# Kernel optimization log

Measured on AMD Instinct MI355X. Metric: run time of the kernel, lower is better.

The kernel has to match this reference:

```python
import jax, jax.numpy as jnp
import numpy as np

B, L, D = 2, 2048, 1024
H, E = 16, 64  # n_heads, per-head dim (E_q=E_k=E_v)
EPS = 1e-5


def _layernorm(x):
    # fresh nn.LayerNorm each forward: gamma=1, beta=0, eps=1e-5 (biased var)
    mu = jnp.mean(x, axis=-1, keepdims=True)
    var = jnp.mean(jnp.square(x - mu), axis=-1, keepdims=True)
    return (x - mu) * jax.lax.rsqrt(var + EPS)


def setup_inputs() -> dict:
    key = jax.random.key(0)
    ks = jax.random.split(key, 9)
    s_in = 1.0 / np.sqrt(D)
    s_ctx = 1.0 / np.sqrt(H * E)
    return {
        "query": jax.random.normal(ks[0], (B, L, D), jnp.float32),
        "key": jax.random.normal(ks[1], (B, L, D), jnp.float32),
        "value": jax.random.normal(ks[2], (B, L, D), jnp.float32),
        # torch nn.Linear weights are [out_features, in_features]
        "W_Q": jax.random.uniform(ks[3], (H * E, D), jnp.float32, -s_in, s_in),
        "W_K": jax.random.uniform(ks[4], (H * E, D), jnp.float32, -s_in, s_in),
        "W_V": jax.random.uniform(ks[5], (H * E, D), jnp.float32, -s_in, s_in),
        "W_O": jax.random.uniform(ks[6], (D, H * E), jnp.float32, -s_ctx, s_ctx),
        "fc_w": jax.random.uniform(ks[7], (D, D), jnp.float32, -s_in, s_in),
        "fc_b": jax.random.uniform(ks[8], (D,), jnp.float32, -s_in, s_in),
    }


def reference(query, key, value, W_Q, W_K, W_V, W_O, fc_w, fc_b):
    b = query.shape[0]
    # projections -> [B, H, L, E]
    q = (query @ W_Q.T).reshape(b, -1, H, E).transpose(0, 2, 1, 3)
    k = (key @ W_K.T).reshape(b, -1, H, E).transpose(0, 2, 1, 3)
    v = (value @ W_V.T).reshape(b, -1, H, E).transpose(0, 2, 1, 3)
    scores = jnp.einsum('bhqe,bhke->bhqk', q, k) / np.sqrt(E).astype(np.float32)
    A = jax.nn.softmax(scores, axis=-1)                 # [B,H,Lq,Lk]
    ctx = jnp.einsum('bhqk,bhke->bhqe', A, v)           # [B,H,L,E]
    ctx = ctx.transpose(0, 2, 1, 3).reshape(b, -1, H * E)
    attn_out = ctx @ W_O.T                               # dropout = identity (eval)
    x = _layernorm(attn_out + query)
    out = x @ fc_w.T + fc_b                              # dropout = identity (eval)
    out = _layernorm(x + out)
    return out
```

## Files before the change

kernel.cpp:

```cpp
#include <hip/hip_runtime.h>
#include <stdint.h>

typedef unsigned short u16;
typedef __bf16 bf16x8 __attribute__((ext_vector_type(8)));
typedef __bf16 bf16x4 __attribute__((ext_vector_type(4)));
typedef float f32x4 __attribute__((ext_vector_type(4)));

#define MFMA16(a,b,c) __builtin_amdgcn_mfma_f32_16x16x32_bf16((a),(b),(c),0,0,0)

__device__ __forceinline__ bf16x4 pack4(float a, float b, float c, float d){
  bf16x4 r; r[0]=(__bf16)a; r[1]=(__bf16)b; r[2]=(__bf16)c; r[3]=(__bf16)d; return r;
}

__device__ __forceinline__ void gl2lds16(const void* g, void* l){
  __builtin_amdgcn_global_load_lds(
      (const __attribute__((address_space(1))) unsigned int*)g,
      (__attribute__((address_space(3))) unsigned int*)l, 16, 0, 0);
}

__device__ __forceinline__ bf16x8 ldsfrag(const u16* base, int row, int gr){
  return *(const bf16x8*)(base + row * 64 + ((gr ^ (row & 7)) << 3));
}

template<int NB, int BN>
__device__ __forceinline__ void gemm_core(const u16* __restrict__ A,
                                          const u16* __restrict__ Bt,
                                          int N, int K, int mode,
                                          void* __restrict__ Cout,
                                          const float* __restrict__ bias,
                                          float oscale)
{
  constexpr int NF = BN / 32;
  __shared__ u16 Al[NB][128 * 64];
  __shared__ u16 Bl[NB][BN * 64];
  const int tid  = threadIdx.x;
  const int lane = tid & 63;
  const int w    = tid >> 6;
  const int wr   = w >> 1, wc = w & 1;
  const int l15  = lane & 15, g = lane >> 4;
  const int rowBase = blockIdx.y << 7;
  const int colBase = blockIdx.x * BN;

  const int srow = tid >> 3;
  const int swz  = ((tid & 7) ^ (srow & 7)) << 3;
  const u16* Ag = A  + (size_t)(rowBase + srow) * K + swz;
  const u16* Bg = Bt + (size_t)(colBase + srow) * K + swz;

  f32x4 acc[4][NF];
#pragma unroll
  for (int m = 0; m < 4; ++m)
#pragma unroll
    for (int n = 0; n < NF; ++n) acc[m][n] = f32x4{0.f, 0.f, 0.f, 0.f};

  auto stage = [&](int buf, int k0) {
#pragma unroll
    for (int i = 0; i < 4; ++i)
      gl2lds16(Ag + (size_t)(i * 32) * K + k0, Al[buf] + i * 2048 + w * 512);
#pragma unroll
    for (int i = 0; i < BN / 32; ++i)
      gl2lds16(Bg + (size_t)(i * 32) * K + k0, Bl[buf] + i * 2048 + w * 512);
  };
  auto compute = [&](int buf) {
    __builtin_amdgcn_s_setprio(1);
#pragma unroll
    for (int kk = 0; kk < 2; ++kk) {
      bf16x8 af[4], bfr[NF];
#pragma unroll
      for (int m = 0; m < 4; ++m) af[m]  = ldsfrag(Al[buf], wr * 64 + m * 16 + l15, kk * 4 + g);
#pragma unroll
      for (int n = 0; n < NF; ++n) bfr[n] = ldsfrag(Bl[buf], wc * (BN/2) + n * 16 + l15, kk * 4 + g);
#pragma unroll
      for (int m = 0; m < 4; ++m)
#pragma unroll
        for (int n = 0; n < NF; ++n)
          acc[m][n] = MFMA16(af[m], bfr[n], acc[m][n]);
    }
    __builtin_amdgcn_s_setprio(0);
  };

  if (NB == 2) {
    stage(0, 0);
    __syncthreads();
    int cur = 0;
    for (int k0 = 0; k0 < K; k0 += 64) {
      if (k0 + 64 < K) stage(cur ^ 1, k0 + 64);
      compute(cur);
      __syncthreads();
      cur ^= 1;
    }
  } else {
    for (int k0 = 0; k0 < K; k0 += 64) {
      stage(0, k0);
      __syncthreads();
      compute(0);
      __syncthreads();
    }
  }

#pragma unroll
  for (int m = 0; m < 4; ++m) {
#pragma unroll
    for (int n = 0; n < NF; ++n) {
      const int row0 = rowBase + wr * 64 + m * 16 + g * 4;
      const int col  = colBase + wc * (BN/2) + n * 16 + l15;
      if (mode == 1) {
        const int b = row0 >> 11, l = row0 & 2047;
        const int h = col >> 6,  e = col & 63;
        *(bf16x4*)((u16*)Cout + ((size_t)((((b << 4) + h) << 6) | e) << 11) + l) =
            pack4(acc[m][n][0], acc[m][n][1], acc[m][n][2], acc[m][n][3]);
      } else {
        const float bb = (mode == 4) ? bias[col] : 0.f;
#pragma unroll
        for (int r = 0; r < 4; ++r) {
          const int row = row0 + r;
          const float v = acc[m][n][r];
          if (mode == 0) {
            *(__bf16*)((u16*)Cout + (size_t)row * N + col) = (__bf16)(v * oscale);
          } else {
            *(__bf16*)((u16*)Cout + (size_t)row * N + col) = (__bf16)(v + bb);
          }
        }
      }
    }
  }
}

#define QSCALE 0.18033688011112042f

__global__ __launch_bounds__(256) void k_proj(
    const u16* __restrict__ qb, const u16* __restrict__ kb, const u16* __restrict__ vb,
    const u16* __restrict__ wq, const u16* __restrict__ wk, const u16* __restrict__ wv,
    u16* __restrict__ Qp, u16* __restrict__ Kp, u16* __restrict__ Vt)
{
  const int z = blockIdx.z;
  const u16* A = (z == 0) ? qb : (z == 1) ? kb : vb;
  const u16* B = (z == 0) ? wq : (z == 1) ? wk : wv;
  void* C = (z == 0) ? (void*)Qp : (z == 1) ? (void*)Kp : (void*)Vt;
  gemm_core<2, 64>(A, B, 1024, 1024, (z == 2) ? 1 : 0, C, nullptr, (z == 0) ? QSCALE : 1.0f);
}

__global__ __launch_bounds__(256) void k_gemm_o(const u16* __restrict__ A,
                                                const u16* __restrict__ B,
                                                u16* __restrict__ C)
{ gemm_core<2, 64>(A, B, 1024, 1024, 0, (void*)C, nullptr, 1.0f); }

__global__ __launch_bounds__(256) void k_gemm_fc(const u16* __restrict__ A,
                                                 const u16* __restrict__ B,
                                                 u16* __restrict__ C,
                                                 const float* __restrict__ bias)
{ gemm_core<2, 64>(A, B, 1024, 1024, 4, (void*)C, bias, 1.0f); }

__global__ __launch_bounds__(256, 2) void k_attn(const u16* __restrict__ Qp,
                                                 const u16* __restrict__ Kp,
                                                 const u16* __restrict__ Vt,
                                                 u16* __restrict__ ctx)
{
  __shared__ u16 Klds[3][64 * 64];
  __shared__ u16 Vlds[3][64 * 64];
  __shared__ u16 Plds[4][32 * 64];

  const int tid = threadIdx.x, lane = tid & 63, w = tid >> 6;
  const int l15 = lane & 15, g = lane >> 4, l7 = l15 & 7;
  const int bh = blockIdx.y, b = bh >> 4, h = bh & 15;
  const int q0 = blockIdx.x << 7;

  bf16x8 bq[2][2];
#pragma unroll
  for (int u = 0; u < 2; ++u) {
    const u16* Qr = Qp + (((size_t)((b << 11) + q0 + (w << 5) + (u << 4) + l15)) << 10)
                  + (h << 6) + (g << 3);
    bq[u][0] = *(const bf16x8*)(Qr);
    bq[u][1] = *(const bf16x8*)(Qr + 32);
  }

  const f32x4 zero4 = {0.f, 0.f, 0.f, 0.f};
  f32x4 o0[4], o1[4];
#pragma unroll
  for (int f = 0; f < 4; ++f) { o0[f] = zero4; o1[f] = zero4; }
  float ds0 = 0.f, ds1 = 0.f;

  const int srow = tid >> 3;
  const int swz  = ((tid & 7) ^ (srow & 7)) << 3;
  const u16* Kg = Kp + (((size_t)((b << 11) + srow)) << 10) + (h << 6) + swz;
  const u16* Vg = Vt + (((size_t)((bh << 6) + srow)) << 11) + swz;
  u16* Pw = Plds[w];

  auto stage = [&](int buf, int j0) {
#pragma unroll
    for (int i = 0; i < 2; ++i) {
      gl2lds16(Kg + ((size_t)(j0 + i * 32) << 10), Klds[buf] + i * 2048 + w * 512);
      gl2lds16(Vg + ((size_t)(i * 32) << 11) + j0, Vlds[buf] + i * 2048 + w * 512);
    }
  };

  stage(0, 0);
  stage(1, 64);
  asm volatile("s_waitcnt vmcnt(4)" ::: "memory");
  __builtin_amdgcn_s_barrier();

  int cur = 0;
  for (int t = 0; t < 32; ++t) {
    if (t + 2 < 32) {
      int nb = cur + 2; if (nb >= 3) nb -= 3;
      stage(nb, (t + 2) << 6);
    }

    bf16x8 kf[4][2];
#pragma unroll
    for (int f = 0; f < 4; ++f) {
      kf[f][0] = ldsfrag(Klds[cur], f * 16 + l15, g);
      kf[f][1] = ldsfrag(Klds[cur], f * 16 + l15, 4 + g);
    }
    f32x4 s0[4], s1[4];
    __builtin_amdgcn_s_setprio(1);
#pragma unroll
    for (int f = 0; f < 4; ++f) {
      s0[f] = MFMA16(kf[f][0], bq[0][0], zero4);
      s0[f] = MFMA16(kf[f][1], bq[0][1], s0[f]);
      s1[f] = MFMA16(kf[f][0], bq[1][0], zero4);
      s1[f] = MFMA16(kf[f][1], bq[1][1], s1[f]);
    }
    __builtin_amdgcn_s_setprio(0);

#pragma unroll
    for (int f = 0; f < 4; ++f) {
      const float a0 = __builtin_amdgcn_exp2f(s0[f][0]);
      const float a1 = __builtin_amdgcn_exp2f(s0[f][1]);
      const float a2 = __builtin_amdgcn_exp2f(s0[f][2]);
      const float a3 = __builtin_amdgcn_exp2f(s0[f][3]);
      ds0 += (a0 + a1) + (a2 + a3);
      *(bf16x4*)(Pw + l15 * 64 + ((((2 * f) + (g >> 1)) ^ l7) << 3) + ((g & 1) << 2)) =
          pack4(a0, a1, a2, a3);
      const float c0 = __builtin_amdgcn_exp2f(s1[f][0]);
      const float c1 = __builtin_amdgcn_exp2f(s1[f][1]);
      const float c2 = __builtin_amdgcn_exp2f(s1[f][2]);
      const float c3 = __builtin_amdgcn_exp2f(s1[f][3]);
      ds1 += (c0 + c1) + (c2 + c3);
      *(bf16x4*)(Pw + (16 + l15) * 64 + ((((2 * f) + (g >> 1)) ^ l7) << 3) + ((g & 1) << 2)) =
          pack4(c0, c1, c2, c3);
    }
    asm volatile("s_waitcnt lgkmcnt(0)" ::: "memory");
    __builtin_amdgcn_sched_barrier(0);

    bf16x8 vf[4][2];
#pragma unroll
    for (int f = 0; f < 4; ++f) {
      vf[f][0] = ldsfrag(Vlds[cur], f * 16 + l15, g);
      vf[f][1] = ldsfrag(Vlds[cur], f * 16 + l15, 4 + g);
    }
    __builtin_amdgcn_s_setprio(1);
#pragma unroll
    for (int kk = 0; kk < 2; ++kk) {
      const bf16x8 pb0 = *(const bf16x8*)(Pw + l15 * 64 + (((kk * 4 + g) ^ l7) << 3));
      const bf16x8 pb1 = *(const bf16x8*)(Pw + (16 + l15) * 64 + (((kk * 4 + g) ^ l7) << 3));
#pragma unroll
      for (int f = 0; f < 4; ++f) {
        o0[f] = MFMA16(vf[f][kk], pb0, o0[f]);
        o1[f] = MFMA16(vf[f][kk], pb1, o1[f]);
      }
    }
    __builtin_amdgcn_s_setprio(0);

    if (t + 2 < 32) {
      asm volatile("s_waitcnt vmcnt(4)" ::: "memory");
      __builtin_amdgcn_s_barrier();
    } else if (t + 1 < 32) {
      asm volatile("s_waitcnt vmcnt(0)" ::: "memory");
      __builtin_amdgcn_s_barrier();
    }
    ++cur; if (cur >= 3) cur -= 3;
  }

  ds0 += __shfl_xor(ds0, 16, 64);
  ds0 += __shfl_xor(ds0, 32, 64);
  ds1 += __shfl_xor(ds1, 16, 64);
  ds1 += __shfl_xor(ds1, 32, 64);
  const float i0 = 1.0f / ds0, i1 = 1.0f / ds1;
  const size_t r0 = (((size_t)((b << 11) + q0 + (w << 5) + l15)) << 10) + (h << 6);
  const size_t r1 = r0 + (16 << 10);
#pragma unroll
  for (int f = 0; f < 4; ++f) {
    *(bf16x4*)(ctx + r0 + f * 16 + (g << 2)) =
        pack4(o0[f][0] * i0, o0[f][1] * i0, o0[f][2] * i0, o0[f][3] * i0);
    *(bf16x4*)(ctx + r1 + f * 16 + (g << 2)) =
        pack4(o1[f][0] * i1, o1[f][1] * i1, o1[f][2] * i1, o1[f][3] * i1);
  }
}

__device__ __forceinline__ void ln_stats(float4 t, int tid, float& mean, float& inv){
  float s = t.x + t.y + t.z + t.w;
  float q = t.x * t.x + t.y * t.y + t.z * t.z + t.w * t.w;
#pragma unroll
  for (int d = 1; d < 64; d <<= 1) {
    s += __shfl_xor(s, d, 64);
    q += __shfl_xor(q, d, 64);
  }
  __shared__ float ps[4], pq[4];
  const int w = tid >> 6;
  if ((tid & 63) == 0) { ps[w] = s; pq[w] = q; }
  __syncthreads();
  s = ps[0] + ps[1] + ps[2] + ps[3];
  q = pq[0] + pq[1] + pq[2] + pq[3];
  mean = s * (1.0f / 1024.0f);
  const float var = q * (1.0f / 1024.0f) - mean * mean;
  inv = rsqrtf(var + 1e-5f);
}

__global__ __launch_bounds__(256) void k_ln1(const u16* __restrict__ a,
                                             const float* __restrict__ res,
                                             u16* __restrict__ xb)
{
  const int row = blockIdx.x, tid = threadIdx.x;
  const size_t base = (size_t)row << 10;
  const bf16x4 av = ((const bf16x4*)(a + base))[tid];
  const float4 rr = ((const float4*)(res + base))[tid];
  float4 t;
  t.x = (float)av[0] + rr.x; t.y = (float)av[1] + rr.y;
  t.z = (float)av[2] + rr.z; t.w = (float)av[3] + rr.w;
  float mean, inv;
  ln_stats(t, tid, mean, inv);
  ((bf16x4*)(xb + base))[tid] = pack4((t.x - mean) * inv, (t.y - mean) * inv,
                                      (t.z - mean) * inv, (t.w - mean) * inv);
}

__global__ __launch_bounds__(256) void k_ln2(const u16* __restrict__ a,
                                             const u16* __restrict__ res,
                                             float* __restrict__ out)
{
  const int row = blockIdx.x, tid = threadIdx.x;
  const size_t base = (size_t)row << 10;
  const bf16x4 av = ((const bf16x4*)(a + base))[tid];
  const bf16x4 rv = ((const bf16x4*)(res + base))[tid];
  float4 t;
  t.x = (float)av[0] + (float)rv[0]; t.y = (float)av[1] + (float)rv[1];
  t.z = (float)av[2] + (float)rv[2]; t.w = (float)av[3] + (float)rv[3];
  float mean, inv;
  ln_stats(t, tid, mean, inv);
  float4 o;
  o.x = (t.x - mean) * inv; o.y = (t.y - mean) * inv;
  o.z = (t.z - mean) * inv; o.w = (t.w - mean) * inv;
  ((float4*)(out + base))[tid] = o;
}

__global__ __launch_bounds__(256) void k_cvt3(const float* __restrict__ q,
                                              const float* __restrict__ k,
                                              const float* __restrict__ v,
                                              u16* __restrict__ qo,
                                              u16* __restrict__ ko,
                                              u16* __restrict__ vo)
{
  const int z = blockIdx.y;
  const float* src = (z == 0) ? q : (z == 1) ? k : v;
  u16* dst = (z == 0) ? qo : (z == 1) ? ko : vo;
  const int i = blockIdx.x * 256 + threadIdx.x;
  const float4 t = ((const float4*)src)[i];
  ((bf16x4*)dst)[i] = pack4(t.x, t.y, t.z, t.w);
}

__global__ __launch_bounds__(256) void k_cvt5(const float* __restrict__ a0,
                                              const float* __restrict__ a1,
                                              const float* __restrict__ a2,
                                              const float* __restrict__ a3,
                                              const float* __restrict__ a4,
                                              u16* __restrict__ o0, u16* __restrict__ o1,
                                              u16* __restrict__ o2, u16* __restrict__ o3,
                                              u16* __restrict__ o4)
{
  const int z = blockIdx.y;
  const float* src = (z == 0) ? a0 : (z == 1) ? a1 : (z == 2) ? a2 : (z == 3) ? a3 : a4;
  u16* dst = (z == 0) ? o0 : (z == 1) ? o1 : (z == 2) ? o2 : (z == 3) ? o3 : o4;
  const int i = blockIdx.x * 256 + threadIdx.x;
  const float4 t = ((const float4*)src)[i];
  ((bf16x4*)dst)[i] = pack4(t.x, t.y, t.z, t.w);
}

extern "C" void kernel_launch(void* const* d_in, const int* in_sizes, int n_in,
                              void* d_out, int out_size, void* d_ws, size_t ws_size,
                              hipStream_t stream)
{
  (void)in_sizes; (void)n_in; (void)out_size; (void)ws_size;
  const float* query = (const float*)d_in[0];
  const float* key   = (const float*)d_in[1];
  const float* value = (const float*)d_in[2];
  const float* W_Q   = (const float*)d_in[3];
  const float* W_K   = (const float*)d_in[4];
  const float* W_V   = (const float*)d_in[5];
  const float* W_O   = (const float*)d_in[6];
  const float* fc_w  = (const float*)d_in[7];
  const float* fc_b  = (const float*)d_in[8];
  float* out = (float*)d_out;
  char* ws = (char*)d_ws;

  u16*   qb    = (u16*)(ws + 0);
  u16*   kb    = (u16*)(ws + 8388608);
  u16*   vb    = (u16*)(ws + 16777216);
  u16*   wq    = (u16*)(ws + 25165824);
  u16*   wk    = (u16*)(ws + 27262976);
  u16*   wv    = (u16*)(ws + 29360128);
  u16*   wo    = (u16*)(ws + 31457280);
  u16*   fw    = (u16*)(ws + 33554432);
  u16*   Qp    = (u16*)(ws + 35651584);
  u16*   Kp    = (u16*)(ws + 44040192);
  u16*   Vt    = (u16*)(ws + 52428800);
  u16*   ctx   = (u16*)(ws + 60817408);
  u16*   attnb = (u16*)(ws + 69206016);
  u16*   xb    = vb;
  u16*   yb    = qb;

  k_cvt3<<<dim3(4096, 3), 256, 0, stream>>>(query, key, value, qb, kb, vb);
  k_cvt5<<<dim3(1024, 5), 256, 0, stream>>>(W_Q, W_K, W_V, W_O, fc_w, wq, wk, wv, wo, fw);
  k_proj<<<dim3(16, 32, 3), 256, 0, stream>>>(qb, kb, vb, wq, wk, wv, Qp, Kp, Vt);
  k_attn<<<dim3(16, 32), 256, 0, stream>>>(Qp, Kp, Vt, ctx);
  k_gemm_o<<<dim3(16, 32), 256, 0, stream>>>(ctx, wo, attnb);
  k_ln1<<<dim3(4096), 256, 0, stream>>>(attnb, query, xb);
  k_gemm_fc<<<dim3(16, 32), 256, 0, stream>>>(xb, fw, yb, fc_b);
  k_ln2<<<dim3(4096), 256, 0, stream>>>(yb, xb, out);
}
```

Before: 156.3 us.

## Split attention over two KV halves with a separate combine kernel

The attention kernel now runs a third grid dimension that splits the 2048 keys into two halves. Each half writes unnormalized fp32 partial outputs and per-row softmax denominators to a workspace buffer. A new combine kernel then sums the halves, normalizes, and writes the bf16 context. K/V staging also drops from triple to double buffering with full __syncthreads, which reduces LDS use. The aim is more blocks in flight and better CU occupancy, at the cost of an extra launch, roughly 32 MB of fp32 partial traffic, and less prefetch depth.

```diff
diff --git a/kernel.cpp b/kernel.cpp
--- a/kernel.cpp
+++ b/kernel.cpp
@@ -153,16 +153,19 @@
 __global__ __launch_bounds__(256, 2) void k_attn(const u16* __restrict__ Qp,
                                                  const u16* __restrict__ Kp,
                                                  const u16* __restrict__ Vt,
-                                                 u16* __restrict__ ctx)
-{
-  __shared__ u16 Klds[3][64 * 64];
-  __shared__ u16 Vlds[3][64 * 64];
+                                                 float* __restrict__ Opart,
+                                                 float* __restrict__ dpart)
+{
+  __shared__ u16 Klds[2][64 * 64];
+  __shared__ u16 Vlds[2][64 * 64];
   __shared__ u16 Plds[4][32 * 64];
 
   const int tid = threadIdx.x, lane = tid & 63, w = tid >> 6;
   const int l15 = lane & 15, g = lane >> 4, l7 = l15 & 7;
   const int bh = blockIdx.y, b = bh >> 4, h = bh & 15;
   const int q0 = blockIdx.x << 7;
+  const int half = blockIdx.z;
+  const int kvbase = half << 10;
 
   bf16x8 bq[2][2];
 #pragma unroll
@@ -181,8 +184,8 @@
 
   const int srow = tid >> 3;
   const int swz  = ((tid & 7) ^ (srow & 7)) << 3;
-  const u16* Kg = Kp + (((size_t)((b << 11) + srow)) << 10) + (h << 6) + swz;
-  const u16* Vg = Vt + (((size_t)((bh << 6) + srow)) << 11) + swz;
+  const u16* Kg = Kp + (((size_t)((b << 11) + kvbase + srow)) << 10) + (h << 6) + swz;
+  const u16* Vg = Vt + (((size_t)((bh << 6) + srow)) << 11) + kvbase + swz;
   u16* Pw = Plds[w];
 
   auto stage = [&](int buf, int j0) {
@@ -194,16 +197,11 @@
   };
 
   stage(0, 0);
-  stage(1, 64);
-  asm volatile("s_waitcnt vmcnt(4)" ::: "memory");
-  __builtin_amdgcn_s_barrier();
-
+  __syncthreads();
   int cur = 0;
-  for (int t = 0; t < 32; ++t) {
-    if (t + 2 < 32) {
-      int nb = cur + 2; if (nb >= 3) nb -= 3;
-      stage(nb, (t + 2) << 6);
-    }
+
+  for (int j0 = 0; j0 < 1024; j0 += 64) {
+    if (j0 + 64 < 1024) stage(cur ^ 1, j0 + 64);
 
     bf16x8 kf[4][2];
 #pragma unroll
@@ -260,31 +258,42 @@
       }
     }
     __builtin_amdgcn_s_setprio(0);
-
-    if (t + 2 < 32) {
-      asm volatile("s_waitcnt vmcnt(4)" ::: "memory");
-      __builtin_amdgcn_s_barrier();
-    } else if (t + 1 < 32) {
-      asm volatile("s_waitcnt vmcnt(0)" ::: "memory");
-      __builtin_amdgcn_s_barrier();
-    }
-    ++cur; if (cur >= 3) cur -= 3;
+    __syncthreads();
+    cur ^= 1;
   }
 
   ds0 += __shfl_xor(ds0, 16, 64);
   ds0 += __shfl_xor(ds0, 32, 64);
   ds1 += __shfl_xor(ds1, 16, 64);
   ds1 += __shfl_xor(ds1, 32, 64);
-  const float i0 = 1.0f / ds0, i1 = 1.0f / ds1;
-  const size_t r0 = (((size_t)((b << 11) + q0 + (w << 5) + l15)) << 10) + (h << 6);
-  const size_t r1 = r0 + (16 << 10);
+
+  const int brow0 = (b << 11) + q0 + (w << 5) + l15;
+  const int brow1 = brow0 + 16;
+  float* Op = Opart + ((size_t)half << 22);
 #pragma unroll
   for (int f = 0; f < 4; ++f) {
-    *(bf16x4*)(ctx + r0 + f * 16 + (g << 2)) =
-        pack4(o0[f][0] * i0, o0[f][1] * i0, o0[f][2] * i0, o0[f][3] * i0);
-    *(bf16x4*)(ctx + r1 + f * 16 + (g << 2)) =
-        pack4(o1[f][0] * i1, o1[f][1] * i1, o1[f][2] * i1, o1[f][3] * i1);
-  }
+    *(f32x4*)(Op + ((size_t)brow0 << 10) + (h << 6) + f * 16 + (g << 2)) = o0[f];
+    *(f32x4*)(Op + ((size_t)brow1 << 10) + (h << 6) + f * 16 + (g << 2)) = o1[f];
+  }
+  if (g == 0) {
+    dpart[(half << 16) + (brow0 << 4) + h] = ds0;
+    dpart[(half << 16) + (brow1 << 4) + h] = ds1;
+  }
+}
+
+__global__ __launch_bounds__(256) void k_combine(const float* __restrict__ Opart,
+                                                 const float* __restrict__ dpart,
+                                                 u16* __restrict__ ctx)
+{
+  const int row = blockIdx.x, tid = threadIdx.x;
+  const int h = tid >> 4;
+  const float d = dpart[(row << 4) + h] + dpart[(1 << 16) + (row << 4) + h];
+  const float inv = 1.0f / d;
+  const f32x4 p0 = ((const f32x4*)(Opart + ((size_t)row << 10)))[tid];
+  const f32x4 p1 = ((const f32x4*)(Opart + (1u << 22) + ((size_t)row << 10)))[tid];
+  ((bf16x4*)(ctx + ((size_t)row << 10)))[tid] =
+      pack4((p0[0] + p1[0]) * inv, (p0[1] + p1[1]) * inv,
+            (p0[2] + p1[2]) * inv, (p0[3] + p1[3]) * inv);
 }
 
 __device__ __forceinline__ void ln_stats(float4 t, int tid, float& mean, float& inv){
@@ -403,6 +412,8 @@
   u16*   Kp    = (u16*)(ws + 44040192);
   u16*   Vt    = (u16*)(ws + 52428800);
   u16*   ctx   = (u16*)(ws + 60817408);
+  float* Opart = (float*)(ws + 69206016);
+  float* dpart = (float*)(ws + 102760448);
   u16*   attnb = (u16*)(ws + 69206016);
   u16*   xb    = vb;
   u16*   yb    = qb;
@@ -410,7 +421,8 @@
   k_cvt3<<<dim3(4096, 3), 256, 0, stream>>>(query, key, value, qb, kb, vb);
   k_cvt5<<<dim3(1024, 5), 256, 0, stream>>>(W_Q, W_K, W_V, W_O, fc_w, wq, wk, wv, wo, fw);
   k_proj<<<dim3(16, 32, 3), 256, 0, stream>>>(qb, kb, vb, wq, wk, wv, Qp, Kp, Vt);
-  k_attn<<<dim3(16, 32), 256, 0, stream>>>(Qp, Kp, Vt, ctx);
+  k_attn<<<dim3(16, 32, 2), 256, 0, stream>>>(Qp, Kp, Vt, Opart, dpart);
+  k_combine<<<dim3(4096), 256, 0, stream>>>(Opart, dpart, ctx);
   k_gemm_o<<<dim3(16, 32), 256, 0, stream>>>(ctx, wo, attnb);
   k_ln1<<<dim3(4096), 256, 0, stream>>>(attnb, query, xb);
   k_gemm_fc<<<dim3(16, 32), 256, 0, stream>>>(xb, fw, yb, fc_b);
```

After: 164.4 us. 1.05x slower.
